# Optimization experiments

Hardware: AMD Instinct MI355X
Metric: run time of the kernel (lower is better)

The kernel has to match this reference:

```python
import jax, jax.numpy as jnp
import numpy as np

B, S, E, H = 4, 2048, 1024, 16
DH = E // H


def setup_inputs() -> dict:
    key = jax.random.key(0)
    ks = jax.random.split(key, 11)
    scale = 1.0 / np.sqrt(E)
    inp = {
        "q": jax.random.normal(ks[0], (B, S, E), jnp.float32),
        "k": jax.random.normal(ks[1], (B, S, E), jnp.float32),
        "v": jax.random.normal(ks[2], (B, S, E), jnp.float32),
        # torch nn.Linear weights: shape [out, in], y = x @ W.T + b
        "wq": jax.random.normal(ks[3], (E, E), jnp.float32) * scale,
        "bq": jnp.zeros((E,), jnp.float32),
        "wk": jax.random.normal(ks[4], (E, E), jnp.float32) * scale,
        "bk": jnp.zeros((E,), jnp.float32),
        "wv": jax.random.normal(ks[5], (E, E), jnp.float32) * scale,
        "bv": jnp.zeros((E,), jnp.float32),
        "wo": jax.random.normal(ks[6], (E, E), jnp.float32) * scale,
        "bo": jnp.zeros((E,), jnp.float32),
        "causal": 1,
    }
    return inp


def reference(q, k, v, wq, bq, wk, bk, wv, bv, wo, bo, causal):
    # Projections (torch Linear: x @ W.T + b)
    Q = q @ wq.T + bq  # [B,S,E]
    K = k @ wk.T + bk
    V = v @ wv.T + bv
    # split heads -> [B,H,S,Dh]
    Q = Q.reshape(B, S, H, DH).transpose(0, 2, 1, 3)
    K = K.reshape(B, S, H, DH).transpose(0, 2, 1, 3)
    V = V.reshape(B, S, H, DH).transpose(0, 2, 1, 3)
    scores = jnp.einsum("bhqd,bhkd->bhqk", Q, K) / np.sqrt(DH)
    if causal:
        cmask = jnp.triu(jnp.ones((S, S), bool), k=1)  # True above diagonal
        scores = jnp.where(cmask[None, None], -jnp.inf, scores)
    attn = jax.nn.softmax(scores, axis=-1)  # [B,H,S,S]
    out = jnp.einsum("bhqk,bhkd->bhqd", attn, V)
    out = out.transpose(0, 2, 1, 3).reshape(B, S, E)
    out = out @ wo.T + bo
    return (out, attn)
```

## Files before the change

### kernel.cpp

```cpp
#include <hip/hip_runtime.h>
#include <hip/hip_bf16.h>

typedef __bf16 bf16;
typedef __bf16 bf16x4 __attribute__((ext_vector_type(4)));
typedef __bf16 bf16x8 __attribute__((ext_vector_type(8)));
typedef float f32x4 __attribute__((ext_vector_type(4)));

constexpr int Bc = 4, Sc = 2048, Ec = 1024, Hc = 16, DHc = 64;
constexpr int MBS = Bc * Sc;
constexpr size_t NE = (size_t)MBS * Ec;
constexpr size_t EE = (size_t)Ec * Ec;

__device__ __forceinline__ void gload16(const bf16* g, bf16* l) {
  __builtin_amdgcn_global_load_lds(
      (const __attribute__((address_space(1))) void*)g,
      (__attribute__((address_space(3))) void*)l, 16, 0, 0);
}

__global__ __launch_bounds__(256) void cvt_all_kernel(
    const float* __restrict__ q, const float* __restrict__ k,
    const float* __restrict__ v, const float* __restrict__ wq,
    const float* __restrict__ wk, const float* __restrict__ wv,
    bf16* __restrict__ qb, bf16* __restrict__ kb, bf16* __restrict__ vb,
    bf16* __restrict__ wqb, bf16* __restrict__ wkb, bf16* __restrict__ wvb)
{
  const int g = blockIdx.x;
  const float* s; bf16* d; size_t off;
  if (g < 12288) {
    const int t = g >> 12;
    s = (t == 0) ? q : (t == 1) ? k : v;
    d = (t == 0) ? qb : (t == 1) ? kb : vb;
    off = (size_t)(g & 4095) * 2048;
  } else {
    const int t = (g - 12288) >> 9;
    s = (t == 0) ? wq : (t == 1) ? wk : wv;
    d = (t == 0) ? wqb : (t == 1) ? wkb : wvb;
    off = (size_t)((g - 12288) & 511) * 2048;
  }
  const size_t i = off + (size_t)threadIdx.x * 8;
  const float4 a = *(const float4*)&s[i];
  const float4 b = *(const float4*)&s[i + 4];
  bf16x8 o = { (bf16)a.x, (bf16)a.y, (bf16)a.z, (bf16)a.w,
               (bf16)b.x, (bf16)b.y, (bf16)b.z, (bf16)b.w };
  *(bf16x8*)&d[i] = o;
}

__global__ __launch_bounds__(256) void cvt_one_kernel(
    const float* __restrict__ s, bf16* __restrict__ d)
{
  const size_t i = (size_t)blockIdx.x * 2048 + (size_t)threadIdx.x * 8;
  const float4 a = *(const float4*)&s[i];
  const float4 b = *(const float4*)&s[i + 4];
  bf16x8 o = { (bf16)a.x, (bf16)a.y, (bf16)a.z, (bf16)a.w,
               (bf16)b.x, (bf16)b.y, (bf16)b.z, (bf16)b.w };
  *(bf16x8*)&d[i] = o;
}

template<bool OUT_BF16>
__global__ __launch_bounds__(256, 2) void gemm_bt_bf16(
    const bf16* __restrict__ A, const bf16* __restrict__ W,
    const float* __restrict__ bias, void* __restrict__ Cout)
{
  __shared__ bf16 As[128][64];
  __shared__ bf16 Ws[128][64];
  const int tid  = threadIdx.x;
  const int wave = tid >> 6, lane = tid & 63;
  const int quad = lane >> 4, l16 = lane & 15;
  const int lr = lane >> 3, lc = lane & 7;
  const int wm = (wave & 1) * 64, wn = (wave >> 1) * 64;
  const int gg = blockIdx.x;
  const int m0 = ((gg & 7) * 8 + ((gg >> 3) >> 3)) * 128;
  const int n0 = ((gg >> 3) & 7) * 128;
  f32x4 acc[4][4] = {};

  for (int k0 = 0; k0 < 1024; k0 += 64) {
    __syncthreads();
#pragma unroll
    for (int c = 0; c < 4; ++c) {
      const int row = wave * 32 + c * 8 + lr;
      gload16(A + (size_t)(m0 + row) * 1024 + k0 + ((lc ^ lr) << 3),
              &As[wave * 32 + c * 8][0]);
      gload16(W + (size_t)(n0 + row) * 1024 + k0 + ((lc ^ lr) << 3),
              &Ws[wave * 32 + c * 8][0]);
    }
    __syncthreads();
#pragma unroll
    for (int kk = 0; kk < 2; ++kk) {
      bf16x8 af[4], bg[4];
#pragma unroll
      for (int i = 0; i < 4; ++i) {
        const int row = wm + i * 16 + l16;
        af[i] = *(const bf16x8*)&As[row][((((kk << 2) + quad) ^ (row & 7)) << 3)];
      }
#pragma unroll
      for (int j = 0; j < 4; ++j) {
        const int row = wn + j * 16 + l16;
        bg[j] = *(const bf16x8*)&Ws[row][((((kk << 2) + quad) ^ (row & 7)) << 3)];
      }
#pragma unroll
      for (int i = 0; i < 4; ++i)
#pragma unroll
        for (int j = 0; j < 4; ++j)
          acc[i][j] = __builtin_amdgcn_mfma_f32_16x16x32_bf16(af[i], bg[j], acc[i][j], 0, 0, 0);
    }
  }

#pragma unroll
  for (int j = 0; j < 4; ++j) {
    const int col = n0 + wn + j * 16 + l16;
    const float bv = bias[col];
#pragma unroll
    for (int i = 0; i < 4; ++i) {
      const int rowb = m0 + wm + i * 16 + quad * 4;
#pragma unroll
      for (int r = 0; r < 4; ++r) {
        const float v = acc[i][j][r] + bv;
        if constexpr (OUT_BF16)
          ((bf16*)Cout)[(size_t)(rowb + r) * 1024 + col] = (bf16)v;
        else
          ((float*)Cout)[(size_t)(rowb + r) * 1024 + col] = v;
      }
    }
  }
}

__global__ __launch_bounds__(256, 2) void fused_attn_kernel(
    const bf16* __restrict__ Qp, const bf16* __restrict__ Kp,
    const bf16* __restrict__ Vp, float* __restrict__ attn,
    bf16* __restrict__ Op)
{
  const int g   = blockIdx.x;
  const int idx = g >> 3;
  const int bh  = (g & 7) * 8 + (idx >> 4);
  const int tr  = 15 - (idx & 15);
  const int b = bh >> 4, h = bh & 15;
  const int row0 = tr * 128;
  float* __restrict__ out = attn + (size_t)bh * Sc * Sc;
  const size_t hoff = (size_t)b * Sc * Ec + (size_t)h * DHc;
  const bf16* __restrict__ Vh = Vp + hoff;
  bf16* __restrict__ Oh = Op + hoff;

  __shared__ bf16 Ks[128][64];
  __shared__ bf16 Ps[128][128];
  __shared__ bf16 Vt[64][136];
  __shared__ float sred[2][2][128];

  const int tid  = threadIdx.x;
  const int wave = tid >> 6, lane = tid & 63;
  const int quad = lane >> 4, l16 = lane & 15;
  const int lr = lane >> 3, lc = lane & 7;
  const int wqm = (wave & 1) * 64;
  const int wkn = (wave >> 1) * 64;
  const int wnO = (wave >> 1) * 32;

  bf16* PsQ = &Ps[0][0];
#pragma unroll
  for (int c = 0; c < 4; ++c) {
    const int row = wave * 32 + c * 8 + lr;
    gload16(Qp + hoff + (size_t)(row0 + row) * Ec + ((lc ^ lr) << 3),
            PsQ + (size_t)(wave * 32 + c * 8) * 64);
  }
  __syncthreads();
  bf16x8 qf[4][2];
#pragma unroll
  for (int i = 0; i < 4; ++i)
#pragma unroll
    for (int kk = 0; kk < 2; ++kk) {
      const int row = wqm + i * 16 + l16;
      qf[i][kk] = *(const bf16x8*)(PsQ + (size_t)row * 64 +
                                   ((((kk << 2) + quad) ^ (row & 7)) << 3));
    }

  float m_r[4], l_r[4];
#pragma unroll
  for (int i = 0; i < 4; ++i) { m_r[i] = -3.4e38f; l_r[i] = 0.f; }

  for (int tc = 0; tc <= tr; ++tc) {
    const int col0 = tc * 128;
    __syncthreads();
#pragma unroll
    for (int c = 0; c < 4; ++c) {
      const int row = wave * 32 + c * 8 + lr;
      gload16(Kp + hoff + (size_t)(col0 + row) * Ec + ((lc ^ lr) << 3),
              &Ks[wave * 32 + c * 8][0]);
    }
    __syncthreads();
    f32x4 sc[4][4] = {};
#pragma unroll
    for (int kk = 0; kk < 2; ++kk) {
      bf16x8 kf[4];
#pragma unroll
      for (int j = 0; j < 4; ++j) {
        const int row = wkn + j * 16 + l16;
        kf[j] = *(const bf16x8*)&Ks[row][((((kk << 2) + quad) ^ (row & 7)) << 3)];
      }
#pragma unroll
      for (int i = 0; i < 4; ++i)
#pragma unroll
        for (int j = 0; j < 4; ++j)
          sc[i][j] = __builtin_amdgcn_mfma_f32_16x16x32_bf16(kf[j], qf[i][kk], sc[i][j], 0, 0, 0);
    }
    if (tc == tr) {
#pragma unroll
      for (int i = 0; i < 4; ++i) {
        const int row_t = wqm + i * 16 + l16;
#pragma unroll
        for (int j = 0; j < 4; ++j) {
          const int colb = wkn + j * 16 + quad * 4;
#pragma unroll
          for (int r = 0; r < 4; ++r)
            if (colb + r > row_t) sc[i][j][r] = -3.4e38f;
        }
      }
    }
#pragma unroll
    for (int i = 0; i < 4; ++i) {
      float tm = sc[i][0][0];
#pragma unroll
      for (int j = 0; j < 4; ++j)
#pragma unroll
        for (int r = 0; r < 4; ++r) tm = fmaxf(tm, sc[i][j][r]);
      tm = fmaxf(tm, __shfl_xor(tm, 16, 64));
      tm = fmaxf(tm, __shfl_xor(tm, 32, 64));
      const float mn = fmaxf(m_r[i], tm);
      float s = 0.f;
#pragma unroll
      for (int j = 0; j < 4; ++j)
#pragma unroll
        for (int r = 0; r < 4; ++r) s += __expf((sc[i][j][r] - mn) * 0.125f);
      s += __shfl_xor(s, 16, 64);
      s += __shfl_xor(s, 32, 64);
      l_r[i] = l_r[i] * __expf((m_r[i] - mn) * 0.125f) + s;
      m_r[i] = mn;
    }
  }

  {
    const int cg = wave >> 1;
    if (quad == 0) {
#pragma unroll
      for (int i = 0; i < 4; ++i) {
        const int row = wqm + i * 16 + l16;
        sred[0][cg][row] = m_r[i];
        sred[1][cg][row] = l_r[i];
      }
    }
    __syncthreads();
#pragma unroll
    for (int i = 0; i < 4; ++i) {
      const int row = wqm + i * 16 + l16;
      const float ma = sred[0][0][row], mb = sred[0][1][row];
      const float la = sred[1][0][row], lb = sred[1][1][row];
      const float mn = fmaxf(ma, mb);
      const float l = la * __expf((ma - mn) * 0.125f)
                    + lb * __expf((mb - mn) * 0.125f);
      m_r[i] = mn;
      l_r[i] = 1.f / l;
    }
  }

  f32x4 oacc[4][2] = {};
  for (int tc = 0; tc <= tr; ++tc) {
    const int col0 = tc * 128;
    const bool diag = (tc == tr);
    __syncthreads();
#pragma unroll
    for (int c = 0; c < 4; ++c) {
      const int row = wave * 32 + c * 8 + lr;
      gload16(Kp + hoff + (size_t)(col0 + row) * Ec + ((lc ^ lr) << 3),
              &Ks[wave * 32 + c * 8][0]);
    }
    {
      const int kk_ = tid >> 1;
      const int nh  = (tid & 1) * 32;
      const bf16* src = Vh + (size_t)(col0 + kk_) * Ec + nh;
#pragma unroll
      for (int u = 0; u < 4; ++u) {
        uint4 raw = *(const uint4*)(src + u * 8);
        const bf16* pv = (const bf16*)&raw;
#pragma unroll
        for (int jj = 0; jj < 8; ++jj) Vt[nh + u * 8 + jj][kk_] = pv[jj];
      }
    }
    __syncthreads();
    f32x4 sc[4][4] = {};
#pragma unroll
    for (int kk = 0; kk < 2; ++kk) {
      bf16x8 kf[4];
#pragma unroll
      for (int j = 0; j < 4; ++j) {
        const int row = wkn + j * 16 + l16;
        kf[j] = *(const bf16x8*)&Ks[row][((((kk << 2) + quad) ^ (row & 7)) << 3)];
      }
#pragma unroll
      for (int i = 0; i < 4; ++i)
#pragma unroll
        for (int j = 0; j < 4; ++j)
          sc[i][j] = __builtin_amdgcn_mfma_f32_16x16x32_bf16(kf[j], qf[i][kk], sc[i][j], 0, 0, 0);
    }
#pragma unroll
    for (int i = 0; i < 4; ++i) {
      const int row_t = wqm + i * 16 + l16;
      float* orow = out + (size_t)(row0 + row_t) * Sc + col0;
      char* pw = (char*)&Ps[0][0] + row_t * 256;
      const int sw = (row_t & 7) << 4;
#pragma unroll
      for (int j = 0; j < 4; ++j) {
        const int colb = wkn + j * 16 + quad * 4;
        f32x4 p4;
#pragma unroll
        for (int r = 0; r < 4; ++r) {
          float p = __expf((sc[i][j][r] - m_r[i]) * 0.125f) * l_r[i];
          if (diag && (colb + r > row_t)) p = 0.f;
          p4[r] = p;
        }
        __builtin_nontemporal_store(p4, (f32x4*)(orow + colb));
        bf16x4 pb = { (bf16)p4[0], (bf16)p4[1], (bf16)p4[2], (bf16)p4[3] };
        *(bf16x4*)(pw + ((colb * 2) ^ sw)) = pb;
      }
    }
    __syncthreads();
#pragma unroll
    for (int c = 0; c < 4; ++c) {
      bf16x8 vf[2], pf[4];
#pragma unroll
      for (int j2 = 0; j2 < 2; ++j2)
        vf[j2] = *(const bf16x8*)&Vt[wnO + j2 * 16 + l16][c * 32 + quad * 8];
#pragma unroll
      for (int i = 0; i < 4; ++i) {
        const int row = wqm + i * 16 + l16;
        pf[i] = *(const bf16x8*)((const char*)&Ps[0][0] + row * 256 +
                                 ((c * 64 + quad * 16) ^ ((row & 7) << 4)));
      }
#pragma unroll
      for (int i = 0; i < 4; ++i)
#pragma unroll
        for (int j2 = 0; j2 < 2; ++j2)
          oacc[i][j2] = __builtin_amdgcn_mfma_f32_16x16x32_bf16(vf[j2], pf[i], oacc[i][j2], 0, 0, 0);
    }
  }

#pragma unroll
  for (int i = 0; i < 4; ++i) {
    const int grow = row0 + wqm + i * 16 + l16;
#pragma unroll
    for (int j2 = 0; j2 < 2; ++j2) {
      const int ncol = wnO + j2 * 16 + quad * 4;
      bf16x4 ov = { (bf16)oacc[i][j2][0], (bf16)oacc[i][j2][1],
                    (bf16)oacc[i][j2][2], (bf16)oacc[i][j2][3] };
      *(bf16x4*)&Oh[(size_t)grow * Ec + ncol] = ov;
    }
  }

  {
    const f32x4 z = {0.f, 0.f, 0.f, 0.f};
    const int rsub = tid >> 5, csub = (tid & 31) * 4;
    for (int tc2 = tr + 1; tc2 < 16; ++tc2) {
      const int col0 = tc2 * 128;
#pragma unroll
      for (int rr = 0; rr < 16; ++rr) {
        const int row = row0 + rr * 8 + rsub;
        __builtin_nontemporal_store(z, (f32x4*)&out[(size_t)row * Sc + col0 + csub]);
      }
    }
  }
}

extern "C" void kernel_launch(void* const* d_in, const int* in_sizes, int n_in,
                              void* d_out, int out_size, void* d_ws, size_t ws_size,
                              hipStream_t stream) {
  (void)in_sizes; (void)n_in; (void)out_size; (void)ws_size;
  const float* q  = (const float*)d_in[0];
  const float* k  = (const float*)d_in[1];
  const float* v  = (const float*)d_in[2];
  const float* wq = (const float*)d_in[3];
  const float* bq = (const float*)d_in[4];
  const float* wk = (const float*)d_in[5];
  const float* bk = (const float*)d_in[6];
  const float* wv = (const float*)d_in[7];
  const float* bv = (const float*)d_in[8];
  const float* wo = (const float*)d_in[9];
  const float* bo = (const float*)d_in[10];

  float* out  = (float*)d_out;
  float* attn = out + NE;

  bf16* wsQ = (bf16*)d_ws;
  bf16* wsK = wsQ + NE;
  bf16* wsV = wsK + NE;
  bf16* wsO = wsV + NE;

  bf16* qb  = (bf16*)attn;
  bf16* kb  = qb + NE;
  bf16* vb  = kb + NE;
  bf16* wqb = vb + NE;
  bf16* wkb = wqb + EE;
  bf16* wvb = wkb + EE;

  cvt_all_kernel<<<13824, 256, 0, stream>>>(q, k, v, wq, wk, wv,
                                            qb, kb, vb, wqb, wkb, wvb);

  gemm_bt_bf16<true><<<512, 256, 0, stream>>>(qb, wqb, bq, wsQ);
  gemm_bt_bf16<true><<<512, 256, 0, stream>>>(kb, wkb, bk, wsK);
  gemm_bt_bf16<true><<<512, 256, 0, stream>>>(vb, wvb, bv, wsV);

  fused_attn_kernel<<<1024, 256, 0, stream>>>(wsQ, wsK, wsV, attn, wsO);

  cvt_one_kernel<<<512, 256, 0, stream>>>(wo, wsQ);
  gemm_bt_bf16<false><<<512, 256, 0, stream>>>(wsO, wsQ, bo, out);
}
```

Baseline: 1.396 ms.

## Double-buffer GEMM and attention K loads, merge projections and conversions into fewer launches

The GEMM is refactored into a shared core that double-buffers A/W tiles in LDS, so the next k-slice loads while MFMAs run. It also swaps MFMA operand order so bias add and stores are vectorized. The three QKV projections become one 1536-block launch, and the Wo conversion folds into the main conversion kernel. The attention kernel double-buffers K tiles in pass one, prefetches V into registers and the next K tile during the second pass, and packs the V transpose into bf16x2 writes. Together these cut launches and exposed load latency, at the cost of doubled LDS for the GEMM and more workspace for the bf16 Wo.

```diff
diff --git a/kernel.cpp b/kernel.cpp
--- a/kernel.cpp
+++ b/kernel.cpp
@@ -2,6 +2,7 @@
 #include <hip/hip_bf16.h>
 
 typedef __bf16 bf16;
+typedef __bf16 bf16x2 __attribute__((ext_vector_type(2)));
 typedef __bf16 bf16x4 __attribute__((ext_vector_type(4)));
 typedef __bf16 bf16x8 __attribute__((ext_vector_type(8)));
 typedef float f32x4 __attribute__((ext_vector_type(4)));
@@ -21,8 +22,10 @@
     const float* __restrict__ q, const float* __restrict__ k,
     const float* __restrict__ v, const float* __restrict__ wq,
     const float* __restrict__ wk, const float* __restrict__ wv,
+    const float* __restrict__ wo,
     bf16* __restrict__ qb, bf16* __restrict__ kb, bf16* __restrict__ vb,
-    bf16* __restrict__ wqb, bf16* __restrict__ wkb, bf16* __restrict__ wvb)
+    bf16* __restrict__ wqb, bf16* __restrict__ wkb, bf16* __restrict__ wvb,
+    bf16* __restrict__ wob)
 {
   const int g = blockIdx.x;
   const float* s; bf16* d; size_t off;
@@ -33,8 +36,8 @@
     off = (size_t)(g & 4095) * 2048;
   } else {
     const int t = (g - 12288) >> 9;
-    s = (t == 0) ? wq : (t == 1) ? wk : wv;
-    d = (t == 0) ? wqb : (t == 1) ? wkb : wvb;
+    s = (t == 0) ? wq : (t == 1) ? wk : (t == 2) ? wv : wo;
+    d = (t == 0) ? wqb : (t == 1) ? wkb : (t == 2) ? wvb : wob;
     off = (size_t)((g - 12288) & 511) * 2048;
   }
   const size_t i = off + (size_t)threadIdx.x * 8;
@@ -45,83 +48,101 @@
   *(bf16x8*)&d[i] = o;
 }
 
-__global__ __launch_bounds__(256) void cvt_one_kernel(
-    const float* __restrict__ s, bf16* __restrict__ d)
+template<bool OUT_BF16>
+__device__ __forceinline__ void gemm_core(
+    const bf16* __restrict__ A, const bf16* __restrict__ W,
+    const float* __restrict__ bias, void* __restrict__ Cout,
+    int gg, bf16 (&As)[2][128][64], bf16 (&Ws)[2][128][64])
 {
-  const size_t i = (size_t)blockIdx.x * 2048 + (size_t)threadIdx.x * 8;
-  const float4 a = *(const float4*)&s[i];
-  const float4 b = *(const float4*)&s[i + 4];
-  bf16x8 o = { (bf16)a.x, (bf16)a.y, (bf16)a.z, (bf16)a.w,
-               (bf16)b.x, (bf16)b.y, (bf16)b.z, (bf16)b.w };
-  *(bf16x8*)&d[i] = o;
-}
-
-template<bool OUT_BF16>
-__global__ __launch_bounds__(256, 2) void gemm_bt_bf16(
-    const bf16* __restrict__ A, const bf16* __restrict__ W,
-    const float* __restrict__ bias, void* __restrict__ Cout)
-{
-  __shared__ bf16 As[128][64];
-  __shared__ bf16 Ws[128][64];
   const int tid  = threadIdx.x;
   const int wave = tid >> 6, lane = tid & 63;
   const int quad = lane >> 4, l16 = lane & 15;
   const int lr = lane >> 3, lc = lane & 7;
   const int wm = (wave & 1) * 64, wn = (wave >> 1) * 64;
-  const int gg = blockIdx.x;
-  const int m0 = ((gg & 7) * 8 + ((gg >> 3) >> 3)) * 128;
+  const int m0 = ((gg & 7) * 8 + (gg >> 6)) * 128;
   const int n0 = ((gg >> 3) & 7) * 128;
   f32x4 acc[4][4] = {};
 
-  for (int k0 = 0; k0 < 1024; k0 += 64) {
-    __syncthreads();
+  auto stage = [&](int buf, int k0) {
 #pragma unroll
     for (int c = 0; c < 4; ++c) {
-      const int row = wave * 32 + c * 8 + lr;
-      gload16(A + (size_t)(m0 + row) * 1024 + k0 + ((lc ^ lr) << 3),
-              &As[wave * 32 + c * 8][0]);
-      gload16(W + (size_t)(n0 + row) * 1024 + k0 + ((lc ^ lr) << 3),
-              &Ws[wave * 32 + c * 8][0]);
-    }
-    __syncthreads();
+      const int row = wave * 32 + c * 8;
+      gload16(A + (size_t)(m0 + row + lr) * 1024 + k0 + ((lc ^ lr) << 3),
+              &As[buf][row][0]);
+      gload16(W + (size_t)(n0 + row + lr) * 1024 + k0 + ((lc ^ lr) << 3),
+              &Ws[buf][row][0]);
+    }
+  };
+
+  stage(0, 0);
+  __syncthreads();
+  for (int t = 0; t < 16; ++t) {
+    const int cur = t & 1;
+    if (t < 15) stage(cur ^ 1, (t + 1) * 64);
 #pragma unroll
     for (int kk = 0; kk < 2; ++kk) {
       bf16x8 af[4], bg[4];
 #pragma unroll
       for (int i = 0; i < 4; ++i) {
         const int row = wm + i * 16 + l16;
-        af[i] = *(const bf16x8*)&As[row][((((kk << 2) + quad) ^ (row & 7)) << 3)];
+        af[i] = *(const bf16x8*)&As[cur][row][((((kk << 2) + quad) ^ (row & 7)) << 3)];
       }
 #pragma unroll
       for (int j = 0; j < 4; ++j) {
         const int row = wn + j * 16 + l16;
-        bg[j] = *(const bf16x8*)&Ws[row][((((kk << 2) + quad) ^ (row & 7)) << 3)];
+        bg[j] = *(const bf16x8*)&Ws[cur][row][((((kk << 2) + quad) ^ (row & 7)) << 3)];
       }
 #pragma unroll
       for (int i = 0; i < 4; ++i)
 #pragma unroll
         for (int j = 0; j < 4; ++j)
-          acc[i][j] = __builtin_amdgcn_mfma_f32_16x16x32_bf16(af[i], bg[j], acc[i][j], 0, 0, 0);
-    }
-  }
-
-#pragma unroll
-  for (int j = 0; j < 4; ++j) {
-    const int col = n0 + wn + j * 16 + l16;
-    const float bv = bias[col];
-#pragma unroll
-    for (int i = 0; i < 4; ++i) {
-      const int rowb = m0 + wm + i * 16 + quad * 4;
-#pragma unroll
-      for (int r = 0; r < 4; ++r) {
-        const float v = acc[i][j][r] + bv;
-        if constexpr (OUT_BF16)
-          ((bf16*)Cout)[(size_t)(rowb + r) * 1024 + col] = (bf16)v;
-        else
-          ((float*)Cout)[(size_t)(rowb + r) * 1024 + col] = v;
-      }
-    }
-  }
+          acc[i][j] = __builtin_amdgcn_mfma_f32_16x16x32_bf16(bg[j], af[i], acc[i][j], 0, 0, 0);
+    }
+    __syncthreads();
+  }
+
+#pragma unroll
+  for (int i = 0; i < 4; ++i) {
+    const int row = m0 + wm + i * 16 + l16;
+#pragma unroll
+    for (int j = 0; j < 4; ++j) {
+      const int colb = n0 + wn + j * 16 + quad * 4;
+      const float4 bv = *(const float4*)&bias[colb];
+      f32x4 v = { acc[i][j][0] + bv.x, acc[i][j][1] + bv.y,
+                  acc[i][j][2] + bv.z, acc[i][j][3] + bv.w };
+      if constexpr (OUT_BF16) {
+        bf16x4 o = { (bf16)v[0], (bf16)v[1], (bf16)v[2], (bf16)v[3] };
+        *(bf16x4*)&((bf16*)Cout)[(size_t)row * 1024 + colb] = o;
+      } else {
+        *(f32x4*)&((float*)Cout)[(size_t)row * 1024 + colb] = v;
+      }
+    }
+  }
+}
+
+__global__ __launch_bounds__(256, 2) void proj3_kernel(
+    const bf16* __restrict__ qb, const bf16* __restrict__ kb,
+    const bf16* __restrict__ vb, const bf16* __restrict__ wqb,
+    const bf16* __restrict__ wkb, const bf16* __restrict__ wvb,
+    const float* __restrict__ bq, const float* __restrict__ bk,
+    const float* __restrict__ bv,
+    bf16* __restrict__ Qo, bf16* __restrict__ Ko, bf16* __restrict__ Vo)
+{
+  __shared__ bf16 As[2][128][64], Ws[2][128][64];
+  const int g = blockIdx.x, which = g >> 9, gg = g & 511;
+  const bf16* A = (which == 0) ? qb : (which == 1) ? kb : vb;
+  const bf16* W = (which == 0) ? wqb : (which == 1) ? wkb : wvb;
+  const float* bias = (which == 0) ? bq : (which == 1) ? bk : bv;
+  bf16* C = (which == 0) ? Qo : (which == 1) ? Ko : Vo;
+  gemm_core<true>(A, W, bias, C, gg, As, Ws);
+}
+
+__global__ __launch_bounds__(256, 2) void gemm_out_kernel(
+    const bf16* __restrict__ A, const bf16* __restrict__ W,
+    const float* __restrict__ bias, float* __restrict__ C)
+{
+  __shared__ bf16 As[2][128][64], Ws[2][128][64];
+  gemm_core<false>(A, W, bias, C, blockIdx.x, As, Ws);
 }
 
 __global__ __launch_bounds__(256, 2) void fused_attn_kernel(
@@ -140,10 +161,11 @@
   const bf16* __restrict__ Vh = Vp + hoff;
   bf16* __restrict__ Oh = Op + hoff;
 
-  __shared__ bf16 Ks[128][64];
-  __shared__ bf16 Ps[128][128];
-  __shared__ bf16 Vt[64][136];
+  __shared__ bf16 KPool[2][8704];
+  __shared__ bf16 Ps[128 * 128];
   __shared__ float sred[2][2][128];
+  bf16* Ks = KPool[0];
+  bf16 (*Vt)[136] = (bf16(*)[136])KPool[1];
 
   const int tid  = threadIdx.x;
   const int wave = tid >> 6, lane = tid & 63;
@@ -153,13 +175,22 @@
   const int wkn = (wave >> 1) * 64;
   const int wnO = (wave >> 1) * 32;
 
-  bf16* PsQ = &Ps[0][0];
+  auto stageK = [&](bf16* dst, int col0_) {
+#pragma unroll
+    for (int c = 0; c < 4; ++c) {
+      const int row = wave * 32 + c * 8;
+      gload16(Kp + hoff + (size_t)(col0_ + row + lr) * Ec + ((lc ^ lr) << 3),
+              dst + row * 64);
+    }
+  };
+
 #pragma unroll
   for (int c = 0; c < 4; ++c) {
-    const int row = wave * 32 + c * 8 + lr;
-    gload16(Qp + hoff + (size_t)(row0 + row) * Ec + ((lc ^ lr) << 3),
-            PsQ + (size_t)(wave * 32 + c * 8) * 64);
-  }
+    const int row = wave * 32 + c * 8;
+    gload16(Qp + hoff + (size_t)(row0 + row + lr) * Ec + ((lc ^ lr) << 3),
+            Ps + row * 64);
+  }
+  stageK(Ks, 0);
   __syncthreads();
   bf16x8 qf[4][2];
 #pragma unroll
@@ -167,7 +198,7 @@
 #pragma unroll
     for (int kk = 0; kk < 2; ++kk) {
       const int row = wqm + i * 16 + l16;
-      qf[i][kk] = *(const bf16x8*)(PsQ + (size_t)row * 64 +
+      qf[i][kk] = *(const bf16x8*)(Ps + row * 64 +
                                    ((((kk << 2) + quad) ^ (row & 7)) << 3));
     }
 
@@ -176,15 +207,8 @@
   for (int i = 0; i < 4; ++i) { m_r[i] = -3.4e38f; l_r[i] = 0.f; }
 
   for (int tc = 0; tc <= tr; ++tc) {
-    const int col0 = tc * 128;
-    __syncthreads();
-#pragma unroll
-    for (int c = 0; c < 4; ++c) {
-      const int row = wave * 32 + c * 8 + lr;
-      gload16(Kp + hoff + (size_t)(col0 + row) * Ec + ((lc ^ lr) << 3),
-              &Ks[wave * 32 + c * 8][0]);
-    }
-    __syncthreads();
+    if (tc < tr) stageK(KPool[(tc & 1) ^ 1], (tc + 1) * 128);
+    const bf16* kb_ = KPool[tc & 1];
     f32x4 sc[4][4] = {};
 #pragma unroll
     for (int kk = 0; kk < 2; ++kk) {
@@ -192,7 +216,8 @@
 #pragma unroll
       for (int j = 0; j < 4; ++j) {
         const int row = wkn + j * 16 + l16;
-        kf[j] = *(const bf16x8*)&Ks[row][((((kk << 2) + quad) ^ (row & 7)) << 3)];
+        kf[j] = *(const bf16x8*)(kb_ + row * 64 +
+                                 ((((kk << 2) + quad) ^ (row & 7)) << 3));
       }
 #pragma unroll
       for (int i = 0; i < 4; ++i)
@@ -233,7 +258,18 @@
       l_r[i] = l_r[i] * __expf((m_r[i] - mn) * 0.125f) + s;
       m_r[i] = mn;
     }
-  }
+    __syncthreads();
+  }
+
+  const int kp = (tid & 63) * 2;
+  const int nh = (tid >> 6) * 16;
+  bf16x8 v0a, v0b, v1a, v1b;
+  {
+    const bf16* s0 = Vh + (size_t)kp * Ec + nh;
+    v0a = *(const bf16x8*)s0;        v0b = *(const bf16x8*)(s0 + 8);
+    v1a = *(const bf16x8*)(s0 + Ec); v1b = *(const bf16x8*)(s0 + Ec + 8);
+  }
+  stageK(Ks, 0);
 
   {
     const int cg = wave >> 1;
@@ -265,24 +301,17 @@
     const bool diag = (tc == tr);
     __syncthreads();
 #pragma unroll
-    for (int c = 0; c < 4; ++c) {
-      const int row = wave * 32 + c * 8 + lr;
-      gload16(Kp + hoff + (size_t)(col0 + row) * Ec + ((lc ^ lr) << 3),
-              &Ks[wave * 32 + c * 8][0]);
-    }
-    {
-      const int kk_ = tid >> 1;
-      const int nh  = (tid & 1) * 32;
-      const bf16* src = Vh + (size_t)(col0 + kk_) * Ec + nh;
-#pragma unroll
-      for (int u = 0; u < 4; ++u) {
-        uint4 raw = *(const uint4*)(src + u * 8);
-        const bf16* pv = (const bf16*)&raw;
-#pragma unroll
-        for (int jj = 0; jj < 8; ++jj) Vt[nh + u * 8 + jj][kk_] = pv[jj];
-      }
-    }
-    __syncthreads();
+    for (int jj = 0; jj < 8; ++jj) {
+      bf16x2 w0 = { v0a[jj], v1a[jj] };
+      *(bf16x2*)&Vt[nh + jj][kp] = w0;
+      bf16x2 w1 = { v0b[jj], v1b[jj] };
+      *(bf16x2*)&Vt[nh + jj + 8][kp] = w1;
+    }
+    if (tc < tr) {
+      const bf16* s0 = Vh + (size_t)(col0 + 128 + kp) * Ec + nh;
+      v0a = *(const bf16x8*)s0;        v0b = *(const bf16x8*)(s0 + 8);
+      v1a = *(const bf16x8*)(s0 + Ec); v1b = *(const bf16x8*)(s0 + Ec + 8);
+    }
     f32x4 sc[4][4] = {};
 #pragma unroll
     for (int kk = 0; kk < 2; ++kk) {
@@ -290,7 +319,8 @@
 #pragma unroll
       for (int j = 0; j < 4; ++j) {
         const int row = wkn + j * 16 + l16;
-        kf[j] = *(const bf16x8*)&Ks[row][((((kk << 2) + quad) ^ (row & 7)) << 3)];
+        kf[j] = *(const bf16x8*)(Ks + row * 64 +
+                                 ((((kk << 2) + quad) ^ (row & 7)) << 3));
       }
 #pragma unroll
       for (int i = 0; i < 4; ++i)
@@ -302,7 +332,7 @@
     for (int i = 0; i < 4; ++i) {
       const int row_t = wqm + i * 16 + l16;
       float* orow = out + (size_t)(row0 + row_t) * Sc + col0;
-      char* pw = (char*)&Ps[0][0] + row_t * 256;
+      char* pw = (char*)Ps + row_t * 256;
       const int sw = (row_t & 7) << 4;
 #pragma unroll
       for (int j = 0; j < 4; ++j) {
@@ -320,6 +350,7 @@
       }
     }
     __syncthreads();
+    if (tc < tr) stageK(Ks, col0 + 128);
 #pragma unroll
     for (int c = 0; c < 4; ++c) {
       bf16x8 vf[2], pf[4];
@@ -329,7 +360,7 @@
 #pragma unroll
       for (int i = 0; i < 4; ++i) {
         const int row = wqm + i * 16 + l16;
-        pf[i] = *(const bf16x8*)((const char*)&Ps[0][0] + row * 256 +
+        pf[i] = *(const bf16x8*)((const char*)Ps + row * 256 +
                                  ((c * 64 + quad * 16) ^ ((row & 7) << 4)));
       }
 #pragma unroll
@@ -389,6 +420,7 @@
   bf16* wsK = wsQ + NE;
   bf16* wsV = wsK + NE;
   bf16* wsO = wsV + NE;
+  bf16* wob = wsO + NE;
 
   bf16* qb  = (bf16*)attn;
   bf16* kb  = qb + NE;
@@ -397,15 +429,13 @@
   bf16* wkb = wqb + EE;
   bf16* wvb = wkb + EE;
 
-  cvt_all_kernel<<<13824, 256, 0, stream>>>(q, k, v, wq, wk, wv,
-                                            qb, kb, vb, wqb, wkb, wvb);
-
-  gemm_bt_bf16<true><<<512, 256, 0, stream>>>(qb, wqb, bq, wsQ);
-  gemm_bt_bf16<true><<<512, 256, 0, stream>>>(kb, wkb, bk, wsK);
-  gemm_bt_bf16<true><<<512, 256, 0, stream>>>(vb, wvb, bv, wsV);
+  cvt_all_kernel<<<14336, 256, 0, stream>>>(q, k, v, wq, wk, wv, wo,
+                                            qb, kb, vb, wqb, wkb, wvb, wob);
+
+  proj3_kernel<<<1536, 256, 0, stream>>>(qb, kb, vb, wqb, wkb, wvb,
+                                         bq, bk, bv, wsQ, wsK, wsV);
 
   fused_attn_kernel<<<1024, 256, 0, stream>>>(wsQ, wsK, wsV, attn, wsO);
 
-  cvt_one_kernel<<<512, 256, 0, stream>>>(wo, wsQ);
-  gemm_bt_bf16<false><<<512, 256, 0, stream>>>(wsO, wsQ, bo, out);
-}
+  gemm_out_kernel<<<512, 256, 0, stream>>>(wsO, wob, bo, out);
+}
```

New measurement: 1.387 ms. Within noise of the previous version (-0.7%).
